# Performance work log

Measured on AMD Instinct MI355X. Metric: run time of the kernel, lower is better.

## Reference

```python
import jax, jax.numpy as jnp
import numpy as np
import math

N, M = 512, 31
INP, EMB, ATT = 64, 64, 64
NUM_RELS = 200
SELF_LOOP_IDX = NUM_RELS  # index num_rels is the self-loop relation


def setup_inputs() -> dict:
    key = jax.random.key(0)
    ks = jax.random.split(key, 11)
    s_w = 1.0 / math.sqrt(EMB)
    return {
        "h": jax.random.normal(ks[0], (N, INP), jnp.float32),
        "msg": jax.random.normal(ks[1], (N, M, EMB), jnp.float32),
        "msg_type": jax.random.randint(ks[2], (N, M), 0, NUM_RELS, jnp.int32),
        "r_label_node": jax.random.randint(ks[3], (N,), 0, NUM_RELS, jnp.int32),
        "r_label_msg": jax.random.randint(ks[4], (N, M), 0, NUM_RELS, jnp.int32),
        "W_self": jax.random.normal(ks[5], (INP, EMB), jnp.float32) * s_w,
        "Q": jax.random.normal(ks[6], (NUM_RELS + 1, EMB, ATT), jnp.float32) * s_w,
        "K": jax.random.normal(ks[7], (NUM_RELS + 1, EMB, ATT), jnp.float32) * s_w,
        "V": jax.random.normal(ks[8], (NUM_RELS + 1, EMB, ATT), jnp.float32) * s_w,
        "ffn_w": jax.random.normal(ks[9], (ATT, EMB), jnp.float32) * s_w,
        "ffn_b": jnp.zeros((EMB,), jnp.float32),
    }


def reference(h, msg, msg_type, r_label_node, r_label_msg, W_self, Q, K, V, ffn_w, ffn_b):
    curr = h @ W_self                                        # [N, EMB]
    x = jnp.concatenate([curr[:, None, :], msg], axis=1)     # [N, M+1, EMB]
    qv_idx = jnp.concatenate([r_label_node[:, None], r_label_msg], axis=1)  # [N, M+1]
    self_col = jnp.full((x.shape[0], 1), SELF_LOOP_IDX, msg_type.dtype)
    k_idx = jnp.concatenate([self_col, msg_type], axis=1)    # [N, M+1]
    # relation-indexed per-token projection weights (irregular gather)
    q = jnp.einsum("nme,nmea->nma", x, Q[qv_idx])            # [N, M+1, ATT]
    k = jnp.einsum("nme,nmea->nma", x, K[k_idx])             # [N, M+1, ATT]
    v = jnp.einsum("nme,nmea->nma", x, V[qv_idx])            # [N, M+1, ATT]
    scores = jnp.einsum("nqa,nka->nqk", q, k) / math.sqrt(ATT)
    # NOTE: original code applies softmax over dim=1 (the query axis)
    att = jax.nn.softmax(scores, axis=1)                     # [N, M+1, M+1]
    pooled = jnp.einsum("nqk,nka->nqa", att, v)[:, 0]        # [N, ATT]
    return pooled @ ffn_w + ffn_b                            # [N, EMB]
```

## Files before the change

### kernel.cpp

```cpp
#include <hip/hip_runtime.h>
#include <math.h>

#define NN 512
#define MM 31
#define TT 32
#define EE 64
#define NREL 200
#define NMAT 201
#define SELF_LOOP 200
#define QCAP 192
#define NT 6
#define WSTR 72
#define CPAD 32

typedef short  short8 __attribute__((ext_vector_type(8)));
typedef float  f32x4  __attribute__((ext_vector_type(4)));

__device__ __forceinline__ unsigned short f2bf(float f) {
    union { float f; unsigned int u; } a; a.f = f;
    unsigned int r = a.u + 0x7FFFu + ((a.u >> 16) & 1u);
    return (unsigned short)(r >> 16);
}

__global__ __launch_bounds__(256) void prep_convert_kernel(
    const float* __restrict__ h, const float* __restrict__ W_self,
    const float* __restrict__ Q, const float* __restrict__ K,
    const float* __restrict__ V,
    const int* __restrict__ msg_type, const int* __restrict__ r_label_node,
    const int* __restrict__ r_label_msg,
    int* __restrict__ cnt_q, int* __restrict__ cnt_k,
    int* __restrict__ list_q, int* __restrict__ list_k,
    unsigned short* __restrict__ wt_q, unsigned short* __restrict__ wt_k,
    unsigned short* __restrict__ wt_v,
    float* __restrict__ curr_all, float* __restrict__ k_all)
{
    const int bid = blockIdx.x, tid = threadIdx.x;

    if (bid < 3 * NMAT) {
        const int r   = bid % NMAT;
        const int mat = bid / NMAT;
        const float* src = (mat == 0 ? Q : mat == 1 ? K : V) + (size_t)r * EE * EE;
        unsigned short* dst = (mat == 0 ? wt_q : mat == 1 ? wt_k : wt_v)
                              + (size_t)r * EE * EE;
        __shared__ unsigned short t_s[EE * WSTR];

        {
            const int e = tid >> 2, aseg = (tid & 3) * 16;
            const float4* s4 = (const float4*)(src + e * EE + aseg);
            float4 f0 = s4[0], f1 = s4[1], f2 = s4[2], f3 = s4[3];
            unsigned short b[16] = {
                f2bf(f0.x), f2bf(f0.y), f2bf(f0.z), f2bf(f0.w),
                f2bf(f1.x), f2bf(f1.y), f2bf(f1.z), f2bf(f1.w),
                f2bf(f2.x), f2bf(f2.y), f2bf(f2.z), f2bf(f2.w),
                f2bf(f3.x), f2bf(f3.y), f2bf(f3.z), f2bf(f3.w) };
            unsigned short* d = &t_s[e * WSTR + aseg];
            *(short8*)d = *(short8*)&b[0];
            *(short8*)(d + 8) = *(short8*)&b[8];
        }
        __syncthreads();
        {
            const int a = tid >> 2, eseg = (tid & 3) * 16;
            unsigned short o[16];
#pragma unroll
            for (int j = 0; j < 16; ++j)
                o[j] = t_s[(eseg + j) * WSTR + a];
            unsigned short* d = dst + a * EE + eseg;
            *(short8*)d = *(short8*)&o[0];
            *(short8*)(d + 8) = *(short8*)&o[8];
        }
        return;
    }

    const int n = bid - 3 * NMAT;

    if (tid < MM) {
        int j  = n * MM + tid;
        int rl = r_label_msg[j];
        int p  = atomicAdd(&cnt_q[rl * CPAD], 1);
        if (p < QCAP) list_q[rl * QCAP + p] = n * TT + tid + 1;
        int mt = msg_type[j];
        int p2 = atomicAdd(&cnt_k[mt * CPAD], 1);
        if (p2 < QCAP) list_k[mt * QCAP + p2] = n * TT + tid + 1;
    } else if (tid == 63) {
        int r = r_label_node[n];
        int p = atomicAdd(&cnt_q[r * CPAD], 1);
        if (p < QCAP) list_q[r * QCAP + p] = n * TT;
    }

    __shared__ float c_s[EE];
    if (tid < EE) {
        const float* hrow = h + n * EE;
        float acc = 0.f;
#pragma unroll 8
        for (int e = 0; e < EE; ++e)
            acc = fmaf(hrow[e], W_self[e * EE + tid], acc);
        curr_all[n * EE + tid] = acc;
        c_s[tid] = acc;
    }
    __syncthreads();
    if (tid < EE) {
        const float* K200 = K + (size_t)SELF_LOOP * EE * EE;
        float k0 = 0.f;
#pragma unroll 8
        for (int e = 0; e < EE; ++e)
            k0 = fmaf(c_s[e], K200[e * EE + tid], k0);
        k_all[(size_t)n * TT * EE + tid] = k0;
    }
}

__global__ __launch_bounds__(256) void proj_tile_kernel(
    const float* __restrict__ curr_all, const float* __restrict__ msg,
    const unsigned short* __restrict__ wt_q,
    const unsigned short* __restrict__ wt_k,
    const unsigned short* __restrict__ wt_v,
    const int* __restrict__ cnt_q, const int* __restrict__ cnt_k,
    const int* __restrict__ list_q, const int* __restrict__ list_k,
    float* __restrict__ q_all, float* __restrict__ k_all,
    float* __restrict__ v_all)
{
    const int r    = blockIdx.x / NT;
    const int tile = blockIdx.x % NT;
    const int tid  = threadIdx.x;
    const int lane = tid & 63;
    const int wave = tid >> 6;
    const int col  = lane & 15;
    const int quad = lane >> 4;

    const int nq = min(cnt_q[r * CPAD], QCAP);
    const int nk = min(cnt_k[r * CPAD], QCAP);
    const int q0 = tile * 32;
    const bool do_q = q0 < nq;
    const bool do_k = q0 < nk;
    if (!do_q && !do_k) return;

    __shared__ unsigned short wq_s[EE * WSTR];
    __shared__ unsigned short wk_s[EE * WSTR];
    __shared__ unsigned short wv_s[EE * WSTR];
    __shared__ unsigned short x_s[64 * WSTR];
    __shared__ int tq_s[32], tk_s[32];

    {
        const int a = tid >> 2, seg = (tid & 3) * 16;
        const size_t go = (size_t)r * EE * EE + a * EE + seg;
        const int lo = a * WSTR + seg;
        if (do_q) {
            short8 w0 = *(const short8*)(wt_q + go);
            short8 w1 = *(const short8*)(wt_q + go + 8);
            *(short8*)&wq_s[lo] = w0; *(short8*)&wq_s[lo + 8] = w1;
            short8 v0 = *(const short8*)(wt_v + go);
            short8 v1 = *(const short8*)(wt_v + go + 8);
            *(short8*)&wv_s[lo] = v0; *(short8*)&wv_s[lo + 8] = v1;
        }
        if (do_k) {
            short8 k0_ = *(const short8*)(wt_k + go);
            short8 k1_ = *(const short8*)(wt_k + go + 8);
            *(short8*)&wk_s[lo] = k0_; *(short8*)&wk_s[lo + 8] = k1_;
        }
    }

    if (tid < 32) {
        tq_s[tid] = (do_q && q0 + tid < nq) ? list_q[r * QCAP + q0 + tid] : -1;
    } else if (tid < 64) {
        int i = tid - 32;
        tk_s[i] = (do_k && q0 + i < nk) ? list_k[r * QCAP + q0 + i] : -1;
    }

    {
        const int row = tid >> 2;
        const int fo  = (tid & 3) * 4;
        const bool qside = row < 32;
        const int li = qside ? (q0 + row) : (q0 + row - 32);
        const bool valid = qside ? (do_q && li < nq) : (do_k && li < nk);
        if (valid) {
            int token = qside ? list_q[r * QCAP + li] : list_k[r * QCAP + li];
            int n = token >> 5, t = token & 31;
            const float* src = (t == 0)
                ? (curr_all + n * EE)
                : (msg + ((size_t)n * MM + (t - 1)) * EE);
            float4 f0 = ((const float4*)src)[fo + 0];
            float4 f1 = ((const float4*)src)[fo + 1];
            float4 f2 = ((const float4*)src)[fo + 2];
            float4 f3 = ((const float4*)src)[fo + 3];
            unsigned short b[16] = {
                f2bf(f0.x), f2bf(f0.y), f2bf(f0.z), f2bf(f0.w),
                f2bf(f1.x), f2bf(f1.y), f2bf(f1.z), f2bf(f1.w),
                f2bf(f2.x), f2bf(f2.y), f2bf(f2.z), f2bf(f2.w),
                f2bf(f3.x), f2bf(f3.y), f2bf(f3.z), f2bf(f3.w) };
            unsigned short* d = &x_s[row * WSTR + fo * 4];
            *(short8*)d       = *(short8*)&b[0];
            *(short8*)(d + 8) = *(short8*)&b[8];
        }
    }
    __syncthreads();

    if (do_q) {
        const int mtile = wave & 1;
        const unsigned short* w_s = (wave >> 1) ? wv_s : wq_s;
        float* outp = (wave >> 1) ? v_all : q_all;
        const int m = mtile * 16 + col;
        f32x4 acc[4] = {{0,0,0,0},{0,0,0,0},{0,0,0,0},{0,0,0,0}};
#pragma unroll
        for (int kk = 0; kk < 2; ++kk) {
            short8 af = *(const short8*)&x_s[m * WSTR + kk * 32 + quad * 8];
#pragma unroll
            for (int nt = 0; nt < 4; ++nt) {
                short8 bf = *(const short8*)&w_s[(nt * 16 + col) * WSTR + kk * 32 + quad * 8];
                acc[nt] = __builtin_amdgcn_mfma_f32_16x16x32_bf16(af, bf, acc[nt], 0, 0, 0);
            }
        }
#pragma unroll
        for (int nt = 0; nt < 4; ++nt)
#pragma unroll
            for (int reg = 0; reg < 4; ++reg) {
                int rrow = mtile * 16 + quad * 4 + reg;
                int token = tq_s[rrow];
                if (token >= 0)
                    outp[(size_t)token * EE + nt * 16 + col] = acc[nt][reg];
            }
    }

    if (do_k) {
        const int mtile = wave & 1;
        const int nh = wave >> 1;
        const int m = 32 + mtile * 16 + col;
        f32x4 acc[2] = {{0,0,0,0},{0,0,0,0}};
#pragma unroll
        for (int kk = 0; kk < 2; ++kk) {
            short8 af = *(const short8*)&x_s[m * WSTR + kk * 32 + quad * 8];
#pragma unroll
            for (int j = 0; j < 2; ++j) {
                int nt = nh * 2 + j;
                short8 bf = *(const short8*)&wk_s[(nt * 16 + col) * WSTR + kk * 32 + quad * 8];
                acc[j] = __builtin_amdgcn_mfma_f32_16x16x32_bf16(af, bf, acc[j], 0, 0, 0);
            }
        }
#pragma unroll
        for (int j = 0; j < 2; ++j)
#pragma unroll
            for (int reg = 0; reg < 4; ++reg) {
                int rrow = mtile * 16 + quad * 4 + reg;
                int token = tk_s[rrow];
                if (token >= 0)
                    k_all[(size_t)token * EE + (nh * 2 + j) * 16 + col] = acc[j][reg];
            }
    }
}

__global__ __launch_bounds__(256) void attn_kernel(
    const float* __restrict__ q_all, const float* __restrict__ k_all,
    const float* __restrict__ v_all, const float* __restrict__ ffn_w,
    const float* __restrict__ ffn_b, float* __restrict__ out)
{
    const int n = blockIdx.x, tid = threadIdx.x;
    __shared__ float q_s[TT][68], k_s[TT][68], v_s[TT][68];
    __shared__ float s_s[TT][TT + 1];
    __shared__ float att0[TT];
    __shared__ float pooled[EE];

    {
        const float4* qg = (const float4*)(q_all + (size_t)n * TT * EE);
        const float4* kg = (const float4*)(k_all + (size_t)n * TT * EE);
        const float4* vg = (const float4*)(v_all + (size_t)n * TT * EE);
        for (int i = tid; i < TT * EE / 4; i += 256) {
            int row = i >> 4, c = i & 15;
            ((float4*)&q_s[row][0])[c] = qg[i];
            ((float4*)&k_s[row][0])[c] = kg[i];
            ((float4*)&v_s[row][0])[c] = vg[i];
        }
    }
    __syncthreads();

    {
        const int ki = tid & 31;
        for (int qi = tid >> 5; qi < TT; qi += 8) {
            const float4* qp = (const float4*)&q_s[qi][0];
            const float4* kp = (const float4*)&k_s[ki][0];
            float acc = 0.f;
            for (int e4 = 0; e4 < EE / 4; ++e4) {
                float4 a = qp[e4], b = kp[e4];
                acc += a.x * b.x + a.y * b.y + a.z * b.z + a.w * b.w;
            }
            s_s[qi][ki] = acc * 0.125f;
        }
    }
    __syncthreads();

    if (tid < TT) {
        float mx = -INFINITY;
        for (int qi = 0; qi < TT; ++qi) mx = fmaxf(mx, s_s[qi][tid]);
        float sum = 0.f;
        for (int qi = 0; qi < TT; ++qi) sum += __expf(s_s[qi][tid] - mx);
        att0[tid] = __expf(s_s[0][tid] - mx) / sum;
    }
    __syncthreads();

    if (tid < EE) {
        float acc = 0.f;
        for (int ki = 0; ki < TT; ++ki)
            acc = fmaf(att0[ki], v_s[ki][tid], acc);
        pooled[tid] = acc;
    }
    __syncthreads();

    if (tid < EE) {
        float acc = ffn_b[tid];
        for (int a = 0; a < EE; ++a)
            acc = fmaf(pooled[a], ffn_w[a * EE + tid], acc);
        out[n * EE + tid] = acc;
    }
}

extern "C" void kernel_launch(void* const* d_in, const int* in_sizes, int n_in,
                              void* d_out, int out_size, void* d_ws, size_t ws_size,
                              hipStream_t stream) {
    const float* h            = (const float*)d_in[0];
    const float* msg          = (const float*)d_in[1];
    const int*   msg_type     = (const int*)  d_in[2];
    const int*   r_label_node = (const int*)  d_in[3];
    const int*   r_label_msg  = (const int*)  d_in[4];
    const float* W_self       = (const float*)d_in[5];
    const float* Q            = (const float*)d_in[6];
    const float* K            = (const float*)d_in[7];
    const float* V            = (const float*)d_in[8];
    const float* ffn_w        = (const float*)d_in[9];
    const float* ffn_b        = (const float*)d_in[10];
    float*       out          = (float*)d_out;

    int* cnt_q  = (int*)d_ws;
    int* cnt_k  = cnt_q + NREL * CPAD;
    int* list_q = cnt_k + NREL * CPAD;
    int* list_k = list_q + NREL * QCAP;
    unsigned short* wt_q = (unsigned short*)(list_k + NREL * QCAP);
    unsigned short* wt_k = wt_q + (size_t)NMAT * EE * EE;
    unsigned short* wt_v = wt_k + (size_t)NMAT * EE * EE;
    float* curr_all = (float*)(wt_v + (size_t)NMAT * EE * EE);
    float* q_all = curr_all + NN * EE;
    float* k_all = q_all + (size_t)NN * TT * EE;
    float* v_all = k_all + (size_t)NN * TT * EE;

    hipMemsetAsync(cnt_q, 0, 2 * NREL * CPAD * sizeof(int), stream);
    prep_convert_kernel<<<3 * NMAT + NN, 256, 0, stream>>>(
        h, W_self, Q, K, V, msg_type, r_label_node, r_label_msg,
        cnt_q, cnt_k, list_q, list_k, wt_q, wt_k, wt_v, curr_all, k_all);
    proj_tile_kernel<<<NREL * NT, 256, 0, stream>>>(
        curr_all, msg, wt_q, wt_k, wt_v, cnt_q, cnt_k, list_q, list_k,
        q_all, k_all, v_all);
    attn_kernel<<<NN, 256, 0, stream>>>(q_all, k_all, v_all, ffn_w, ffn_b, out);
}
```

Baseline: 108.7 us.

## Store intermediates q/k/v and inputs as bf16 to halve global traffic

Converts msg and curr to bf16 once in the prep kernel so the projection kernel gathers bf16 rows instead of fp32 and reconverting. Projection outputs q, k, v are written as bf16, and the attention kernel reads them as bf16 and expands them to fp32 in shared memory. This roughly halves the bytes for the large intermediate buffers passed between kernels. In exchange, the prep kernel gains an extra full pass over msg, and the attention inputs lose precision.

```diff
diff --git a/kernel.cpp b/kernel.cpp
--- a/kernel.cpp
+++ b/kernel.cpp
@@ -21,18 +21,23 @@
     unsigned int r = a.u + 0x7FFFu + ((a.u >> 16) & 1u);
     return (unsigned short)(r >> 16);
 }
+__device__ __forceinline__ float bf2f(unsigned short u) {
+    union { unsigned int u; float f; } a; a.u = ((unsigned int)u) << 16;
+    return a.f;
+}
 
 __global__ __launch_bounds__(256) void prep_convert_kernel(
     const float* __restrict__ h, const float* __restrict__ W_self,
     const float* __restrict__ Q, const float* __restrict__ K,
     const float* __restrict__ V,
     const int* __restrict__ msg_type, const int* __restrict__ r_label_node,
-    const int* __restrict__ r_label_msg,
+    const int* __restrict__ r_label_msg, const float* __restrict__ msg,
     int* __restrict__ cnt_q, int* __restrict__ cnt_k,
     int* __restrict__ list_q, int* __restrict__ list_k,
     unsigned short* __restrict__ wt_q, unsigned short* __restrict__ wt_k,
     unsigned short* __restrict__ wt_v,
-    float* __restrict__ curr_all, float* __restrict__ k_all)
+    unsigned short* __restrict__ msg_bf, unsigned short* __restrict__ curr_bf,
+    unsigned short* __restrict__ k_bf)
 {
     const int bid = blockIdx.x, tid = threadIdx.x;
 
@@ -43,7 +48,6 @@
         unsigned short* dst = (mat == 0 ? wt_q : mat == 1 ? wt_k : wt_v)
                               + (size_t)r * EE * EE;
         __shared__ unsigned short t_s[EE * WSTR];
-
         {
             const int e = tid >> 2, aseg = (tid & 3) * 16;
             const float4* s4 = (const float4*)(src + e * EE + aseg);
@@ -87,6 +91,14 @@
         if (p < QCAP) list_q[r * QCAP + p] = n * TT;
     }
 
+    if (tid < MM * EE / 8) {
+        const float4* s4 = (const float4*)(msg + (size_t)n * MM * EE) + tid * 2;
+        float4 f0 = s4[0], f1 = s4[1];
+        unsigned short b[8] = { f2bf(f0.x), f2bf(f0.y), f2bf(f0.z), f2bf(f0.w),
+                                f2bf(f1.x), f2bf(f1.y), f2bf(f1.z), f2bf(f1.w) };
+        *(short8*)(msg_bf + (size_t)n * MM * EE + tid * 8) = *(short8*)b;
+    }
+
     __shared__ float c_s[EE];
     if (tid < EE) {
         const float* hrow = h + n * EE;
@@ -94,7 +106,7 @@
 #pragma unroll 8
         for (int e = 0; e < EE; ++e)
             acc = fmaf(hrow[e], W_self[e * EE + tid], acc);
-        curr_all[n * EE + tid] = acc;
+        curr_bf[n * EE + tid] = f2bf(acc);
         c_s[tid] = acc;
     }
     __syncthreads();
@@ -104,19 +116,20 @@
 #pragma unroll 8
         for (int e = 0; e < EE; ++e)
             k0 = fmaf(c_s[e], K200[e * EE + tid], k0);
-        k_all[(size_t)n * TT * EE + tid] = k0;
+        k_bf[(size_t)n * TT * EE + tid] = f2bf(k0);
     }
 }
 
 __global__ __launch_bounds__(256) void proj_tile_kernel(
-    const float* __restrict__ curr_all, const float* __restrict__ msg,
+    const unsigned short* __restrict__ curr_bf,
+    const unsigned short* __restrict__ msg_bf,
     const unsigned short* __restrict__ wt_q,
     const unsigned short* __restrict__ wt_k,
     const unsigned short* __restrict__ wt_v,
     const int* __restrict__ cnt_q, const int* __restrict__ cnt_k,
     const int* __restrict__ list_q, const int* __restrict__ list_k,
-    float* __restrict__ q_all, float* __restrict__ k_all,
-    float* __restrict__ v_all)
+    unsigned short* __restrict__ q_bf, unsigned short* __restrict__ k_bf,
+    unsigned short* __restrict__ v_bf)
 {
     const int r    = blockIdx.x / NT;
     const int tile = blockIdx.x % NT;
@@ -167,28 +180,20 @@
 
     {
         const int row = tid >> 2;
-        const int fo  = (tid & 3) * 4;
+        const int seg = (tid & 3) * 16;
         const bool qside = row < 32;
         const int li = qside ? (q0 + row) : (q0 + row - 32);
         const bool valid = qside ? (do_q && li < nq) : (do_k && li < nk);
         if (valid) {
             int token = qside ? list_q[r * QCAP + li] : list_k[r * QCAP + li];
             int n = token >> 5, t = token & 31;
-            const float* src = (t == 0)
-                ? (curr_all + n * EE)
-                : (msg + ((size_t)n * MM + (t - 1)) * EE);
-            float4 f0 = ((const float4*)src)[fo + 0];
-            float4 f1 = ((const float4*)src)[fo + 1];
-            float4 f2 = ((const float4*)src)[fo + 2];
-            float4 f3 = ((const float4*)src)[fo + 3];
-            unsigned short b[16] = {
-                f2bf(f0.x), f2bf(f0.y), f2bf(f0.z), f2bf(f0.w),
-                f2bf(f1.x), f2bf(f1.y), f2bf(f1.z), f2bf(f1.w),
-                f2bf(f2.x), f2bf(f2.y), f2bf(f2.z), f2bf(f2.w),
-                f2bf(f3.x), f2bf(f3.y), f2bf(f3.z), f2bf(f3.w) };
-            unsigned short* d = &x_s[row * WSTR + fo * 4];
-            *(short8*)d       = *(short8*)&b[0];
-            *(short8*)(d + 8) = *(short8*)&b[8];
+            const unsigned short* src = (t == 0)
+                ? (curr_bf + n * EE)
+                : (msg_bf + ((size_t)n * MM + (t - 1)) * EE);
+            short8 s0 = *(const short8*)(src + seg);
+            short8 s1 = *(const short8*)(src + seg + 8);
+            unsigned short* d = &x_s[row * WSTR + seg];
+            *(short8*)d = s0; *(short8*)(d + 8) = s1;
         }
     }
     __syncthreads();
@@ -196,7 +201,7 @@
     if (do_q) {
         const int mtile = wave & 1;
         const unsigned short* w_s = (wave >> 1) ? wv_s : wq_s;
-        float* outp = (wave >> 1) ? v_all : q_all;
+        unsigned short* outp = (wave >> 1) ? v_bf : q_bf;
         const int m = mtile * 16 + col;
         f32x4 acc[4] = {{0,0,0,0},{0,0,0,0},{0,0,0,0},{0,0,0,0}};
 #pragma unroll
@@ -215,7 +220,7 @@
                 int rrow = mtile * 16 + quad * 4 + reg;
                 int token = tq_s[rrow];
                 if (token >= 0)
-                    outp[(size_t)token * EE + nt * 16 + col] = acc[nt][reg];
+                    outp[(size_t)token * EE + nt * 16 + col] = f2bf(acc[nt][reg]);
             }
     }
 
@@ -241,15 +246,17 @@
                 int rrow = mtile * 16 + quad * 4 + reg;
                 int token = tk_s[rrow];
                 if (token >= 0)
-                    k_all[(size_t)token * EE + (nh * 2 + j) * 16 + col] = acc[j][reg];
+                    k_bf[(size_t)token * EE + (nh * 2 + j) * 16 + col] = f2bf(acc[j][reg]);
             }
     }
 }
 
 __global__ __launch_bounds__(256) void attn_kernel(
-    const float* __restrict__ q_all, const float* __restrict__ k_all,
-    const float* __restrict__ v_all, const float* __restrict__ ffn_w,
-    const float* __restrict__ ffn_b, float* __restrict__ out)
+    const unsigned short* __restrict__ q_bf,
+    const unsigned short* __restrict__ k_bf,
+    const unsigned short* __restrict__ v_bf,
+    const float* __restrict__ ffn_w, const float* __restrict__ ffn_b,
+    float* __restrict__ out)
 {
     const int n = blockIdx.x, tid = threadIdx.x;
     __shared__ float q_s[TT][68], k_s[TT][68], v_s[TT][68];
@@ -258,14 +265,16 @@
     __shared__ float pooled[EE];
 
     {
-        const float4* qg = (const float4*)(q_all + (size_t)n * TT * EE);
-        const float4* kg = (const float4*)(k_all + (size_t)n * TT * EE);
-        const float4* vg = (const float4*)(v_all + (size_t)n * TT * EE);
-        for (int i = tid; i < TT * EE / 4; i += 256) {
-            int row = i >> 4, c = i & 15;
-            ((float4*)&q_s[row][0])[c] = qg[i];
-            ((float4*)&k_s[row][0])[c] = kg[i];
-            ((float4*)&v_s[row][0])[c] = vg[i];
+        const int row = tid >> 3, c8 = (tid & 7) * 8;
+        const size_t go = (size_t)n * TT * EE + row * EE + c8;
+        short8 q8 = *(const short8*)(q_bf + go);
+        short8 k8 = *(const short8*)(k_bf + go);
+        short8 v8 = *(const short8*)(v_bf + go);
+#pragma unroll
+        for (int j = 0; j < 8; ++j) {
+            q_s[row][c8 + j] = bf2f(((unsigned short*)&q8)[j]);
+            k_s[row][c8 + j] = bf2f(((unsigned short*)&k8)[j]);
+            v_s[row][c8 + j] = bf2f(((unsigned short*)&v8)[j]);
         }
     }
     __syncthreads();
@@ -333,17 +342,19 @@
     unsigned short* wt_q = (unsigned short*)(list_k + NREL * QCAP);
     unsigned short* wt_k = wt_q + (size_t)NMAT * EE * EE;
     unsigned short* wt_v = wt_k + (size_t)NMAT * EE * EE;
-    float* curr_all = (float*)(wt_v + (size_t)NMAT * EE * EE);
-    float* q_all = curr_all + NN * EE;
-    float* k_all = q_all + (size_t)NN * TT * EE;
-    float* v_all = k_all + (size_t)NN * TT * EE;
+    unsigned short* msg_bf  = wt_v + (size_t)NMAT * EE * EE;
+    unsigned short* curr_bf = msg_bf + (size_t)NN * MM * EE;
+    unsigned short* q_bf = curr_bf + NN * EE;
+    unsigned short* k_bf = q_bf + (size_t)NN * TT * EE;
+    unsigned short* v_bf = k_bf + (size_t)NN * TT * EE;
 
     hipMemsetAsync(cnt_q, 0, 2 * NREL * CPAD * sizeof(int), stream);
     prep_convert_kernel<<<3 * NMAT + NN, 256, 0, stream>>>(
-        h, W_self, Q, K, V, msg_type, r_label_node, r_label_msg,
-        cnt_q, cnt_k, list_q, list_k, wt_q, wt_k, wt_v, curr_all, k_all);
+        h, W_self, Q, K, V, msg_type, r_label_node, r_label_msg, msg,
+        cnt_q, cnt_k, list_q, list_k, wt_q, wt_k, wt_v,
+        msg_bf, curr_bf, k_bf);
     proj_tile_kernel<<<NREL * NT, 256, 0, stream>>>(
-        curr_all, msg, wt_q, wt_k, wt_v, cnt_q, cnt_k, list_q, list_k,
-        q_all, k_all, v_all);
-    attn_kernel<<<NN, 256, 0, stream>>>(q_all, k_all, v_all, ffn_w, ffn_b, out);
-}
+        curr_bf, msg_bf, wt_q, wt_k, wt_v, cnt_q, cnt_k, list_q, list_k,
+        q_bf, k_bf, v_bf);
+    attn_kernel<<<NN, 256, 0, stream>>>(q_bf, k_bf, v_bf, ffn_w, ffn_b, out);
+}
```

New measurement: 107.7 us (median of 2 runs). About the same (-1.0%).
